# Kernel optimization log

Hardware: AMD Instinct MI355X
Metric: run time of the kernel (lower is better)

Reference implementation:

```python
import jax, jax.numpy as jnp
import numpy as np

B, N, E, H, ET = 1, 50000, 600000, 128, 8
EPS = 1e-5


def setup_inputs() -> dict:
    key = jax.random.key(0)
    ks = jax.random.split(key, 20)
    s = 1.0 / np.sqrt(H)
    s2 = 1.0 / np.sqrt(2 * H)
    u = lambda k, shape, b: jax.random.uniform(k, shape, jnp.float32, -b, b)
    return {
        "hidden": jax.random.normal(ks[0], (B, N, H), jnp.float32),
        "edge_index": jax.random.randint(ks[1], (2, E), 0, N),
        "edge_type": jax.random.randint(ks[2], (E,), 0, ET),
        "edge_emb": jax.random.normal(ks[3], (ET, H), jnp.float32),
        "Wq": u(ks[4], (H, H), s), "bq": u(ks[5], (H,), s),
        "Wk": u(ks[6], (H, H), s), "bk": u(ks[7], (H,), s),
        "Wv": u(ks[8], (H, H), s), "bv": u(ks[9], (H,), s),
        "Web": u(ks[10], (H, 1), s), "beb": u(ks[11], (1,), s),
        "W1": u(ks[12], (2 * H, H), s2), "b1": u(ks[13], (H,), s2),
        "W2": u(ks[14], (H, H), s), "b2": u(ks[15], (H,), s),
        "gamma": jnp.ones((H,), jnp.float32),
        "beta": jnp.zeros((H,), jnp.float32),
    }


def reference(hidden, edge_index, edge_type, edge_emb, Wq, bq, Wk, bk, Wv, bv,
              Web, beb, W1, b1, W2, b2, gamma, beta):
    source, target = edge_index[0], edge_index[1]
    src_h = hidden[:, source]                      # [B,E,H] gather
    tgt_h = hidden[:, target]                      # [B,E,H] gather
    eh = edge_emb[edge_type]                       # [E,H]

    q = tgt_h @ Wq + bq                            # [B,E,H]
    sk = src_h + eh[None]                          # [B,E,H]
    k = sk @ Wk + bk
    v = sk @ Wv + bv

    logits = (q * k).sum(-1) / np.sqrt(H)          # [B,E]
    logits = logits + (eh @ Web + beb)[:, 0][None] # edge bias, same across batch

    # segment softmax over incoming edges per target node
    lt = logits.T                                  # [E,B]
    mx = jax.ops.segment_max(lt, target, num_segments=N)   # [N,B]
    ex = jnp.exp(lt - mx[target])
    sm = jax.ops.segment_sum(ex, target, num_segments=N)   # [N,B]
    w = (ex / sm[target]).T                        # [B,E]

    messages = v * w[..., None]                    # [B,E,H]
    agg = jax.ops.segment_sum(jnp.moveaxis(messages, 1, 0), target,
                              num_segments=N)      # [N,B,H]
    agg = jnp.moveaxis(agg, 0, 1)                  # [B,N,H]

    h = jnp.concatenate([hidden, agg], axis=-1)    # [B,N,2H]
    upd = jax.nn.silu(h @ W1 + b1) @ W2 + b2

    x = hidden + upd
    mu = x.mean(-1, keepdims=True)
    var = ((x - mu) ** 2).mean(-1, keepdims=True)
    return (x - mu) / jnp.sqrt(var + EPS) * gamma + beta
```

## Files before the change

### kernel.cpp

```cpp
#include <hip/hip_runtime.h>
#include <math.h>

#define NN 50000
#define NPAD 50048
#define NTILES 3128
#define NE 600000
#define H 128
#define ET 8
#define EPS 1e-5f
#define INVSQ 0.08838834764831845f

typedef __attribute__((ext_vector_type(8))) short bf16x8;
typedef __attribute__((ext_vector_type(8))) unsigned short u16x8;
typedef __attribute__((ext_vector_type(4))) float f32x4;

static __device__ inline float bf_lo(unsigned int w) { return __uint_as_float(w << 16); }
static __device__ inline float bf_hi(unsigned int w) { return __uint_as_float(w & 0xFFFF0000u); }
static __device__ inline float bfu(unsigned short v) {
  return __uint_as_float((unsigned int)v << 16);
}
static __device__ inline unsigned short f2bf(float f) {
  unsigned int u = __float_as_uint(f);
  return (unsigned short)((u + 0x7FFFu + ((u >> 16) & 1u)) >> 16);
}

#define PH_B 3125
#define PW_B 384
#define ET_B 8
#define HIST_B 2344

__global__ __launch_bounds__(256) void prep_all_kernel(
    const float* __restrict__ hidden, const float* __restrict__ edge_emb,
    const float* __restrict__ Wq, const float* __restrict__ Wk, const float* __restrict__ Wv,
    const float* __restrict__ W1, const float* __restrict__ W2,
    const float* __restrict__ Web, const float* __restrict__ beb,
    const int* __restrict__ tgt,
    unsigned short* __restrict__ hcat, unsigned short* __restrict__ WqkvT,
    unsigned short* __restrict__ W1T, unsigned short* __restrict__ W2T,
    float* __restrict__ Kef, float* __restrict__ Vef, float* __restrict__ ebuf,
    int* __restrict__ deg) {
  const int blk = blockIdx.x;
  const int t = threadIdx.x;
  if (blk < PH_B) {
    int g = blk * 256 + t;
    int row = g >> 4, seg = g & 15;
    const float4* src = (const float4*)(hidden + (size_t)row * 128 + seg * 8);
    float4 x0 = src[0], x1 = src[1];
    u16x8 o;
    o[0] = f2bf(x0.x); o[1] = f2bf(x0.y); o[2] = f2bf(x0.z); o[3] = f2bf(x0.w);
    o[4] = f2bf(x1.x); o[5] = f2bf(x1.y); o[6] = f2bf(x1.z); o[7] = f2bf(x1.w);
    *(u16x8*)(hcat + (size_t)row * 256 + seg * 8) = o;
  } else if (blk < PH_B + PW_B) {
    int idx = (blk - PH_B) * 256 + t;
    if (idx < 49152) {
      int r = idx >> 7, k = idx & 127;
      const float* W = (r < 128) ? Wq : (r < 256) ? Wk : Wv;
      WqkvT[idx] = f2bf(W[k * 128 + (r & 127)]);
    } else if (idx < 81920) {
      int j = idx - 49152;
      int r = j >> 8, k = j & 255;
      W1T[j] = f2bf(W1[k * 128 + r]);
    } else if (idx < 98304) {
      int j = idx - 81920;
      int r = j >> 7, k = j & 127;
      W2T[j] = f2bf(W2[k * 128 + r]);
    }
  } else if (blk < PH_B + PW_B + ET_B) {
    int e = blk - (PH_B + PW_B);
    if (t < 128) {
      float sk = 0.f, sv = 0.f;
      for (int i = 0; i < 128; ++i) {
        float ev = edge_emb[e * 128 + i];
        sk = fmaf(ev, Wk[i * 128 + t], sk);
        sv = fmaf(ev, Wv[i * 128 + t], sv);
      }
      Kef[e * 128 + t] = sk;
      Vef[e * 128 + t] = sv;
    } else if (t == 128) {
      float s2 = beb[0];
      for (int i = 0; i < 128; ++i) s2 = fmaf(edge_emb[e * 128 + i], Web[i], s2);
      ebuf[e] = s2;
    }
  } else {
    int e = (blk - (PH_B + PW_B + ET_B)) * 256 + t;
    if (e < NE) atomicAdd(&deg[tgt[e]], 1);
  }
}

__global__ __launch_bounds__(512) void qkv_mfma_kernel(
    const unsigned short* __restrict__ hcat, const unsigned short* __restrict__ WqkvT,
    const float* __restrict__ bq, const float* __restrict__ bk, const float* __restrict__ bv,
    unsigned short* __restrict__ Qb, unsigned short* __restrict__ KV_u16) {
  __shared__ unsigned short stage[64][392];
  const int tid = threadIdx.x;
  const int w = tid >> 6, l = tid & 63;
  const int wr = w >> 2, wc = w & 3;
  const int lr = l & 15, lg = l >> 4;
  const int blk = blockIdx.x;

  f32x4 acc[2][6] = {};
  const unsigned short* Ab = hcat + (size_t)(blk * 64 + wr * 32 + lr) * 256 + lg * 8;
  const unsigned short* Bb = WqkvT + (size_t)(wc * 96 + lr) * 128 + lg * 8;
#pragma unroll
  for (int ks = 0; ks < 4; ++ks) {
    bf16x8 a0 = *(const bf16x8*)(Ab + ks * 32);
    bf16x8 a1 = *(const bf16x8*)(Ab + 16 * 256 + ks * 32);
#pragma unroll
    for (int ct = 0; ct < 6; ++ct) {
      bf16x8 b = *(const bf16x8*)(Bb + ct * 16 * 128 + ks * 32);
      acc[0][ct] = __builtin_amdgcn_mfma_f32_16x16x32_bf16(a0, b, acc[0][ct], 0, 0, 0);
      acc[1][ct] = __builtin_amdgcn_mfma_f32_16x16x32_bf16(a1, b, acc[1][ct], 0, 0, 0);
    }
  }
#pragma unroll
  for (int ct = 0; ct < 6; ++ct) {
    int c = wc * 96 + ct * 16 + lr;
    float bias = (c < 128) ? bq[c] : (c < 256) ? bk[c - 128] : bv[c - 256];
    float sc = (c < 128) ? INVSQ : 1.f;
    int off;
    if (c < 128) off = c;
    else if (c < 256) { int j = c - 128; off = 128 + ((j >> 1) << 2) + (j & 1); }
    else { int j = c - 256; off = 128 + ((j >> 1) << 2) + 2 + (j & 1); }
#pragma unroll
    for (int mt = 0; mt < 2; ++mt)
#pragma unroll
      for (int j = 0; j < 4; ++j)
        stage[wr * 32 + mt * 16 + lg * 4 + j][off] = f2bf((acc[mt][ct][j] + bias) * sc);
  }
  __syncthreads();
  for (int idx = tid; idx < 64 * 48; idx += 512) {
    int r = idx / 48, g = idx % 48;
    int row = blk * 64 + r;
    if (row >= NN) continue;
    u16x8 v = *(const u16x8*)(&stage[r][g * 8]);
    if (g < 16) *(u16x8*)(Qb + (size_t)row * 128 + g * 8) = v;
    else *(u16x8*)(KV_u16 + (size_t)row * 256 + (g - 16) * 8) = v;
  }
}

__global__ __launch_bounds__(256) void qke_kernel(const unsigned short* __restrict__ Qb,
                                                  const float* __restrict__ Kef,
                                                  const float* __restrict__ ebuf,
                                                  float* __restrict__ qke) {
  const int wid = (blockIdx.x * 256 + threadIdx.x) >> 6;
  const int lane = threadIdx.x & 63;
  const int et = lane >> 3, part = lane & 7;
  const unsigned short* q = Qb + (size_t)wid * 128 + part * 16;
  u16x8 q0 = *(const u16x8*)q;
  u16x8 q1 = *(const u16x8*)(q + 8);
  const float4* kf = (const float4*)(Kef + et * 128 + part * 16);
  float4 k0 = kf[0], k1 = kf[1], k2 = kf[2], k3 = kf[3];
  float d = 0.f;
  d = fmaf(bfu(q0[0]), k0.x, d); d = fmaf(bfu(q0[1]), k0.y, d);
  d = fmaf(bfu(q0[2]), k0.z, d); d = fmaf(bfu(q0[3]), k0.w, d);
  d = fmaf(bfu(q0[4]), k1.x, d); d = fmaf(bfu(q0[5]), k1.y, d);
  d = fmaf(bfu(q0[6]), k1.z, d); d = fmaf(bfu(q0[7]), k1.w, d);
  d = fmaf(bfu(q1[0]), k2.x, d); d = fmaf(bfu(q1[1]), k2.y, d);
  d = fmaf(bfu(q1[2]), k2.z, d); d = fmaf(bfu(q1[3]), k2.w, d);
  d = fmaf(bfu(q1[4]), k3.x, d); d = fmaf(bfu(q1[5]), k3.y, d);
  d = fmaf(bfu(q1[6]), k3.z, d); d = fmaf(bfu(q1[7]), k3.w, d);
#pragma unroll
  for (int o = 4; o >= 1; o >>= 1) d += __shfl_xor(d, o);
  if (part == 0) qke[(size_t)wid * 8 + et] = d + ebuf[et];
}

__global__ __launch_bounds__(256) void scan1_kernel(const int* __restrict__ deg,
                                                    int* __restrict__ excl,
                                                    int* __restrict__ sums) {
  __shared__ int buf[256];
  int idx = blockIdx.x * 256 + threadIdx.x;
  int v = (idx < NN) ? deg[idx] : 0;
  buf[threadIdx.x] = v;
  __syncthreads();
  for (int o = 1; o < 256; o <<= 1) {
    int tv = (threadIdx.x >= o) ? buf[threadIdx.x - o] : 0;
    __syncthreads();
    buf[threadIdx.x] += tv;
    __syncthreads();
  }
  if (idx < NN) excl[idx] = buf[threadIdx.x] - v;
  if (threadIdx.x == 255) sums[blockIdx.x] = buf[255];
}

__global__ __launch_bounds__(256) void scan2_kernel(int* __restrict__ sums, int nb) {
  __shared__ int buf[256];
  int v = (threadIdx.x < nb) ? sums[threadIdx.x] : 0;
  buf[threadIdx.x] = v;
  __syncthreads();
  for (int o = 1; o < 256; o <<= 1) {
    int tv = (threadIdx.x >= o) ? buf[threadIdx.x - o] : 0;
    __syncthreads();
    buf[threadIdx.x] += tv;
    __syncthreads();
  }
  if (threadIdx.x < nb) sums[threadIdx.x] = buf[threadIdx.x] - v;
}

__global__ __launch_bounds__(256) void scan3_kernel(const int* __restrict__ excl,
                                                    const int* __restrict__ sums,
                                                    int* __restrict__ row_off,
                                                    int* __restrict__ cursor) {
  int idx = blockIdx.x * 256 + threadIdx.x;
  if (idx < NN) {
    int r = excl[idx] + sums[blockIdx.x];
    row_off[idx] = r;
    cursor[idx] = r;
  }
  if (idx == 0) row_off[NN] = NE;
}

__global__ void scatter_kernel(const int* __restrict__ src, const int* __restrict__ tgt,
                               const int* __restrict__ et, int* __restrict__ cursor,
                               int* __restrict__ packed) {
  int e = blockIdx.x * blockDim.x + threadIdx.x;
  if (e < NE) {
    int pos = atomicAdd(&cursor[tgt[e]], 1);
    packed[pos] = src[e] | (et[e] << 16);
  }
}

__global__ __launch_bounds__(256) void attn_kernel(
    const unsigned short* __restrict__ Qb, const uint4* __restrict__ KV4,
    const float* __restrict__ qke, const float* __restrict__ Vef,
    const int* __restrict__ row_off, const int* __restrict__ packed,
    unsigned short* __restrict__ hcat_u16) {
  const int wid = (blockIdx.x * blockDim.x + threadIdx.x) >> 6;
  const int lane = threadIdx.x & 63;
  const int g = lane >> 4, m = lane & 15;
  const int beg = row_off[wid], end = row_off[wid + 1];
  u16x8 qv = *(const u16x8*)(Qb + (size_t)wid * 128 + m * 8);
  float q[8];
#pragma unroll
  for (int j = 0; j < 8; ++j) q[j] = bfu(qv[j]);
  const float* qkb = qke + (size_t)wid * 8;
  float a[8] = {0.f, 0.f, 0.f, 0.f, 0.f, 0.f, 0.f, 0.f};
  float s = 0.f;
  for (int i = beg; i < end; i += 4) {
    int ii = i + g;
    bool valid = ii < end;
    int p = packed[valid ? ii : beg];
    int src = p & 0xFFFF, et = p >> 16;
    const uint4* row = KV4 + (size_t)src * 32 + m * 2;
    uint4 x0 = row[0], x1 = row[1];
    float d;
    d = bf_lo(x0.x) * q[0];
    d = fmaf(bf_hi(x0.x), q[1], d);
    d = fmaf(bf_lo(x0.z), q[2], d);
    d = fmaf(bf_hi(x0.z), q[3], d);
    d = fmaf(bf_lo(x1.x), q[4], d);
    d = fmaf(bf_hi(x1.x), q[5], d);
    d = fmaf(bf_lo(x1.z), q[6], d);
    d = fmaf(bf_hi(x1.z), q[7], d);
#pragma unroll
    for (int o = 8; o >= 1; o >>= 1) d += __shfl_xor(d, o);
    float pe = __expf(d + qkb[et]);
    pe = valid ? pe : 0.f;
    s += pe;
    const float4* vef = (const float4*)(Vef + et * 128 + m * 8);
    float4 v0 = vef[0], v1 = vef[1];
    a[0] = fmaf(pe, bf_lo(x0.y) + v0.x, a[0]);
    a[1] = fmaf(pe, bf_hi(x0.y) + v0.y, a[1]);
    a[2] = fmaf(pe, bf_lo(x0.w) + v0.z, a[2]);
    a[3] = fmaf(pe, bf_hi(x0.w) + v0.w, a[3]);
    a[4] = fmaf(pe, bf_lo(x1.y) + v1.x, a[4]);
    a[5] = fmaf(pe, bf_hi(x1.y) + v1.y, a[5]);
    a[6] = fmaf(pe, bf_lo(x1.w) + v1.z, a[6]);
    a[7] = fmaf(pe, bf_hi(x1.w) + v1.w, a[7]);
  }
#pragma unroll
  for (int o = 16; o <= 32; o <<= 1) {
    s += __shfl_xor(s, o);
#pragma unroll
    for (int j = 0; j < 8; ++j) a[j] += __shfl_xor(a[j], o);
  }
  if (g == 0) {
    float inv = (s > 0.f) ? 1.f / s : 0.f;
    u16x8 o;
#pragma unroll
    for (int j = 0; j < 8; ++j) o[j] = f2bf(a[j] * inv);
    *(u16x8*)(hcat_u16 + (size_t)wid * 256 + 128 + m * 8) = o;
  }
}

__global__ __launch_bounds__(512) void ffn_mfma_kernel(
    const unsigned short* __restrict__ hcat, const float* __restrict__ hidden,
    const unsigned short* __restrict__ W1T, const unsigned short* __restrict__ W2T,
    const float* __restrict__ b1, const float* __restrict__ b2,
    const float* __restrict__ gamma, const float* __restrict__ beta,
    float* __restrict__ out) {
  __shared__ unsigned short w1s[32768];
  __shared__ unsigned short w2s[16384];
  __shared__ unsigned short mids[8][2176];
  const int tid = threadIdx.x;
  const int w = tid >> 6, l = tid & 63;
  const int lr = l & 15, lg = l >> 4;

#pragma unroll
  for (int it = 0; it < 8; ++it) {
    int idx = it * 512 + tid;
    int c = idx >> 5, ks8 = idx & 31;
    u16x8 v = *(const u16x8*)(W1T + c * 256 + ks8 * 8);
    int byte = (c * 512 + ks8 * 16) ^ ((c & 7) << 4);
    *(u16x8*)((char*)w1s + byte) = v;
  }
#pragma unroll
  for (int it = 0; it < 4; ++it) {
    int idx = it * 512 + tid;
    int c = idx >> 4, ks8 = idx & 15;
    u16x8 v = *(const u16x8*)(W2T + c * 128 + ks8 * 8);
    int byte = (c * 256 + ks8 * 16) ^ ((c & 7) << 4);
    *(u16x8*)((char*)w2s + byte) = v;
  }
  __syncthreads();

  float bias1[8], bias2[8], ga[8], be[8];
#pragma unroll
  for (int ct = 0; ct < 8; ++ct) {
    int c = ct * 16 + lr;
    bias1[ct] = b1[c];
    bias2[ct] = b2[c];
    ga[ct] = gamma[c];
    be[ct] = beta[c];
  }
  unsigned short* midw = mids[w];
  const char* w1b = (const char*)w1s;
  const char* w2b = (const char*)w2s;

  for (int t = blockIdx.x * 8 + w; t < NTILES; t += 2048) {
    const unsigned short* Ab = hcat + (size_t)(t * 16 + lr) * 256 + lg * 8;
    bf16x8 a[8];
#pragma unroll
    for (int ks = 0; ks < 8; ++ks) a[ks] = *(const bf16x8*)(Ab + ks * 32);

    f32x4 acc[8] = {};
#pragma unroll
    for (int ks = 0; ks < 8; ++ks) {
#pragma unroll
      for (int ct = 0; ct < 8; ++ct) {
        int byte = ((ct * 16 + lr) * 512 + (lg * 8 + ks * 32) * 2) ^ ((lr & 7) << 4);
        bf16x8 b = *(const bf16x8*)(w1b + byte);
        acc[ct] = __builtin_amdgcn_mfma_f32_16x16x32_bf16(a[ks], b, acc[ct], 0, 0, 0);
      }
    }

    float res[8][4];
#pragma unroll
    for (int ct = 0; ct < 8; ++ct)
#pragma unroll
      for (int j = 0; j < 4; ++j) {
        int r = t * 16 + lg * 4 + j;
        res[ct][j] = (r < NN) ? hidden[(size_t)r * 128 + ct * 16 + lr] : 0.f;
      }

#pragma unroll
    for (int ct = 0; ct < 8; ++ct) {
      float bb = bias1[ct];
#pragma unroll
      for (int j = 0; j < 4; ++j) {
        float x = acc[ct][j] + bb;
        float sl = x / (1.f + __expf(-x));
        midw[(lg * 4 + j) * 136 + ct * 16 + lr] = f2bf(sl);
      }
    }
    asm volatile("s_waitcnt lgkmcnt(0)" ::: "memory");
    __builtin_amdgcn_sched_barrier(0);

    f32x4 acc2[8] = {};
#pragma unroll
    for (int ks = 0; ks < 4; ++ks) {
      bf16x8 a2 = *(const bf16x8*)(midw + lr * 136 + lg * 8 + ks * 32);
#pragma unroll
      for (int ct = 0; ct < 8; ++ct) {
        int byte = ((ct * 16 + lr) * 256 + (lg * 8 + ks * 32) * 2) ^ ((lr & 7) << 4);
        bf16x8 b = *(const bf16x8*)(w2b + byte);
        acc2[ct] = __builtin_amdgcn_mfma_f32_16x16x32_bf16(a2, b, acc2[ct], 0, 0, 0);
      }
    }

    float x[8][4];
#pragma unroll
    for (int ct = 0; ct < 8; ++ct)
#pragma unroll
      for (int j = 0; j < 4; ++j) x[ct][j] = acc2[ct][j] + bias2[ct] + res[ct][j];
#pragma unroll
    for (int j = 0; j < 4; ++j) {
      float s = 0.f, ss = 0.f;
#pragma unroll
      for (int ct = 0; ct < 8; ++ct) {
        s += x[ct][j];
        ss += x[ct][j] * x[ct][j];
      }
#pragma unroll
      for (int o = 8; o >= 1; o >>= 1) {
        s += __shfl_xor(s, o);
        ss += __shfl_xor(ss, o);
      }
      float mu = s * (1.f / 128.f);
      float inv = rsqrtf(ss * (1.f / 128.f) - mu * mu + EPS);
      int r = t * 16 + lg * 4 + j;
      if (r < NN) {
#pragma unroll
        for (int ct = 0; ct < 8; ++ct) {
          int c = ct * 16 + lr;
          out[(size_t)r * 128 + c] = (x[ct][j] - mu) * inv * ga[ct] + be[ct];
        }
      }
    }
  }
}

extern "C" void kernel_launch(void* const* d_in, const int* in_sizes, int n_in,
                              void* d_out, int out_size, void* d_ws, size_t ws_size,
                              hipStream_t stream) {
  const float* hidden = (const float*)d_in[0];
  const int* edge_index = (const int*)d_in[1];
  const int* edge_type = (const int*)d_in[2];
  const float* edge_emb = (const float*)d_in[3];
  const float* Wq = (const float*)d_in[4];
  const float* bq = (const float*)d_in[5];
  const float* Wk = (const float*)d_in[6];
  const float* bk = (const float*)d_in[7];
  const float* Wv = (const float*)d_in[8];
  const float* bv = (const float*)d_in[9];
  const float* Web = (const float*)d_in[10];
  const float* beb = (const float*)d_in[11];
  const float* W1 = (const float*)d_in[12];
  const float* b1 = (const float*)d_in[13];
  const float* W2 = (const float*)d_in[14];
  const float* b2 = (const float*)d_in[15];
  const float* gamma = (const float*)d_in[16];
  const float* beta = (const float*)d_in[17];
  float* out = (float*)d_out;

  const int* srcp = edge_index;
  const int* tgtp = edge_index + NE;

  size_t off = 0;
  auto alloc = [&](size_t bytes) {
    void* p = (char*)d_ws + off;
    off += (bytes + 255) & ~(size_t)255;
    return p;
  };
  unsigned short* hcat = (unsigned short*)alloc((size_t)NPAD * 256 * 2);
  unsigned short* Qb = (unsigned short*)alloc((size_t)NPAD * 128 * 2);
  unsigned short* KV = (unsigned short*)alloc((size_t)NPAD * 256 * 2);
  unsigned short* WqkvT = (unsigned short*)alloc(384 * 128 * 2);
  unsigned short* W1T = (unsigned short*)alloc(128 * 256 * 2);
  unsigned short* W2T = (unsigned short*)alloc(128 * 128 * 2);
  float* Kef = (float*)alloc(ET * H * 4);
  float* Vef = (float*)alloc(ET * H * 4);
  float* ebuf = (float*)alloc(ET * 4);
  float* qke = (float*)alloc((size_t)NN * 8 * 4);
  int* deg = (int*)alloc((size_t)NN * 4);
  int* excl = (int*)alloc((size_t)NN * 4);
  int* sums = (int*)alloc(256 * 4);
  int* row_off = (int*)alloc((size_t)(NN + 1) * 4);
  int* cursor = (int*)alloc((size_t)NN * 4);
  int* packed = (int*)alloc((size_t)NE * 4);

  hipMemsetAsync(deg, 0, (size_t)NN * 4, stream);

  const int scan_blocks = (NN + 255) / 256;

  prep_all_kernel<<<PH_B + PW_B + ET_B + HIST_B, 256, 0, stream>>>(
      hidden, edge_emb, Wq, Wk, Wv, W1, W2, Web, beb, tgtp, hcat, WqkvT, W1T, W2T, Kef, Vef,
      ebuf, deg);
  scan1_kernel<<<scan_blocks, 256, 0, stream>>>(deg, excl, sums);
  scan2_kernel<<<1, 256, 0, stream>>>(sums, scan_blocks);
  scan3_kernel<<<scan_blocks, 256, 0, stream>>>(excl, sums, row_off, cursor);
  scatter_kernel<<<(NE + 255) / 256, 256, 0, stream>>>(srcp, tgtp, edge_type, cursor, packed);
  qkv_mfma_kernel<<<NPAD / 64, 512, 0, stream>>>(hcat, WqkvT, bq, bk, bv, Qb, KV);
  qke_kernel<<<NN / 4, 256, 0, stream>>>(Qb, Kef, ebuf, qke);
  attn_kernel<<<(NN * 64) / 256, 256, 0, stream>>>(Qb, (const uint4*)KV, qke, Vef, row_off,
                                                   packed, hcat);
  ffn_mfma_kernel<<<256, 512, 0, stream>>>(hcat, hidden, W1T, W2T, b1, b2, gamma, beta, out);
}
```

Measured before the change: 296.7 us.

## Fuse qke into QKV kernel, unroll attention edges by two, widen FFN blocks

Computes the per-node q·Kef edge-type dot products inside the QKV MFMA kernel from the staged Q tile in shared memory, removing the separate qke launch and its Q reload. The attention loop now handles two edge groups per iteration so more gathers are in flight. The FFN kernel goes from 8 to 12 waves per block, with grid-stride and weight-load loops adjusted to match. Risks include higher register pressure in attention, lower occupancy for the 768-thread FFN block given its large LDS footprint, and a scalar per-thread Kef loop that is not vectorised.

After: 340.9 us. 1.15x slower.

```diff
diff --git a/kernel.cpp b/kernel.cpp
--- a/kernel.cpp
+++ b/kernel.cpp
@@ -90,7 +90,9 @@
 __global__ __launch_bounds__(512) void qkv_mfma_kernel(
     const unsigned short* __restrict__ hcat, const unsigned short* __restrict__ WqkvT,
     const float* __restrict__ bq, const float* __restrict__ bk, const float* __restrict__ bv,
-    unsigned short* __restrict__ Qb, unsigned short* __restrict__ KV_u16) {
+    const float* __restrict__ Kef, const float* __restrict__ ebuf,
+    unsigned short* __restrict__ Qb, unsigned short* __restrict__ KV_u16,
+    float* __restrict__ qke) {
   __shared__ unsigned short stage[64][392];
   const int tid = threadIdx.x;
   const int w = tid >> 6, l = tid & 63;
@@ -136,32 +138,22 @@
     if (g < 16) *(u16x8*)(Qb + (size_t)row * 128 + g * 8) = v;
     else *(u16x8*)(KV_u16 + (size_t)row * 256 + (g - 16) * 8) = v;
   }
-}
-
-__global__ __launch_bounds__(256) void qke_kernel(const unsigned short* __restrict__ Qb,
-                                                  const float* __restrict__ Kef,
-                                                  const float* __restrict__ ebuf,
-                                                  float* __restrict__ qke) {
-  const int wid = (blockIdx.x * 256 + threadIdx.x) >> 6;
-  const int lane = threadIdx.x & 63;
-  const int et = lane >> 3, part = lane & 7;
-  const unsigned short* q = Qb + (size_t)wid * 128 + part * 16;
-  u16x8 q0 = *(const u16x8*)q;
-  u16x8 q1 = *(const u16x8*)(q + 8);
-  const float4* kf = (const float4*)(Kef + et * 128 + part * 16);
-  float4 k0 = kf[0], k1 = kf[1], k2 = kf[2], k3 = kf[3];
-  float d = 0.f;
-  d = fmaf(bfu(q0[0]), k0.x, d); d = fmaf(bfu(q0[1]), k0.y, d);
-  d = fmaf(bfu(q0[2]), k0.z, d); d = fmaf(bfu(q0[3]), k0.w, d);
-  d = fmaf(bfu(q0[4]), k1.x, d); d = fmaf(bfu(q0[5]), k1.y, d);
-  d = fmaf(bfu(q0[6]), k1.z, d); d = fmaf(bfu(q0[7]), k1.w, d);
-  d = fmaf(bfu(q1[0]), k2.x, d); d = fmaf(bfu(q1[1]), k2.y, d);
-  d = fmaf(bfu(q1[2]), k2.z, d); d = fmaf(bfu(q1[3]), k2.w, d);
-  d = fmaf(bfu(q1[4]), k3.x, d); d = fmaf(bfu(q1[5]), k3.y, d);
-  d = fmaf(bfu(q1[6]), k3.z, d); d = fmaf(bfu(q1[7]), k3.w, d);
-#pragma unroll
-  for (int o = 4; o >= 1; o >>= 1) d += __shfl_xor(d, o);
-  if (part == 0) qke[(size_t)wid * 8 + et] = d + ebuf[et];
+  {
+    int row = tid >> 3, et = tid & 7;
+    int node = blk * 64 + row;
+    if (node < NN) {
+      const float* kf = Kef + et * 128;
+      const unsigned short* qs = &stage[row][0];
+      float d = 0.f;
+#pragma unroll 16
+      for (int c = 0; c < 128; c += 2) {
+        unsigned int w2 = *(const unsigned int*)(qs + c);
+        d = fmaf(bf_lo(w2), kf[c], d);
+        d = fmaf(bf_hi(w2), kf[c + 1], d);
+      }
+      qke[(size_t)node * 8 + et] = d + ebuf[et];
+    }
+  }
 }
 
 __global__ __launch_bounds__(256) void scan1_kernel(const int* __restrict__ deg,
@@ -235,37 +227,64 @@
   const float* qkb = qke + (size_t)wid * 8;
   float a[8] = {0.f, 0.f, 0.f, 0.f, 0.f, 0.f, 0.f, 0.f};
   float s = 0.f;
-  for (int i = beg; i < end; i += 4) {
-    int ii = i + g;
-    bool valid = ii < end;
-    int p = packed[valid ? ii : beg];
-    int src = p & 0xFFFF, et = p >> 16;
-    const uint4* row = KV4 + (size_t)src * 32 + m * 2;
-    uint4 x0 = row[0], x1 = row[1];
-    float d;
-    d = bf_lo(x0.x) * q[0];
-    d = fmaf(bf_hi(x0.x), q[1], d);
-    d = fmaf(bf_lo(x0.z), q[2], d);
-    d = fmaf(bf_hi(x0.z), q[3], d);
-    d = fmaf(bf_lo(x1.x), q[4], d);
-    d = fmaf(bf_hi(x1.x), q[5], d);
-    d = fmaf(bf_lo(x1.z), q[6], d);
-    d = fmaf(bf_hi(x1.z), q[7], d);
-#pragma unroll
-    for (int o = 8; o >= 1; o >>= 1) d += __shfl_xor(d, o);
-    float pe = __expf(d + qkb[et]);
-    pe = valid ? pe : 0.f;
-    s += pe;
-    const float4* vef = (const float4*)(Vef + et * 128 + m * 8);
-    float4 v0 = vef[0], v1 = vef[1];
-    a[0] = fmaf(pe, bf_lo(x0.y) + v0.x, a[0]);
-    a[1] = fmaf(pe, bf_hi(x0.y) + v0.y, a[1]);
-    a[2] = fmaf(pe, bf_lo(x0.w) + v0.z, a[2]);
-    a[3] = fmaf(pe, bf_hi(x0.w) + v0.w, a[3]);
-    a[4] = fmaf(pe, bf_lo(x1.y) + v1.x, a[4]);
-    a[5] = fmaf(pe, bf_hi(x1.y) + v1.y, a[5]);
-    a[6] = fmaf(pe, bf_lo(x1.w) + v1.z, a[6]);
-    a[7] = fmaf(pe, bf_hi(x1.w) + v1.w, a[7]);
+  for (int i = beg; i < end; i += 8) {
+    int iA = i + g, iB = i + 4 + g;
+    bool vA = iA < end, vB = iB < end;
+    int pA = packed[vA ? iA : beg];
+    int pB = packed[vB ? iB : beg];
+    int sA = pA & 0xFFFF, eA = pA >> 16;
+    int sB = pB & 0xFFFF, eB = pB >> 16;
+    const uint4* rowA = KV4 + (size_t)sA * 32 + m * 2;
+    const uint4* rowB = KV4 + (size_t)sB * 32 + m * 2;
+    uint4 xA0 = rowA[0], xA1 = rowA[1];
+    uint4 xB0 = rowB[0], xB1 = rowB[1];
+    float dA, dB;
+    dA = bf_lo(xA0.x) * q[0];
+    dB = bf_lo(xB0.x) * q[0];
+    dA = fmaf(bf_hi(xA0.x), q[1], dA);
+    dB = fmaf(bf_hi(xB0.x), q[1], dB);
+    dA = fmaf(bf_lo(xA0.z), q[2], dA);
+    dB = fmaf(bf_lo(xB0.z), q[2], dB);
+    dA = fmaf(bf_hi(xA0.z), q[3], dA);
+    dB = fmaf(bf_hi(xB0.z), q[3], dB);
+    dA = fmaf(bf_lo(xA1.x), q[4], dA);
+    dB = fmaf(bf_lo(xB1.x), q[4], dB);
+    dA = fmaf(bf_hi(xA1.x), q[5], dA);
+    dB = fmaf(bf_hi(xB1.x), q[5], dB);
+    dA = fmaf(bf_lo(xA1.z), q[6], dA);
+    dB = fmaf(bf_lo(xB1.z), q[6], dB);
+    dA = fmaf(bf_hi(xA1.z), q[7], dA);
+    dB = fmaf(bf_hi(xB1.z), q[7], dB);
+#pragma unroll
+    for (int o = 8; o >= 1; o >>= 1) {
+      dA += __shfl_xor(dA, o);
+      dB += __shfl_xor(dB, o);
+    }
+    float peA = __expf(dA + qkb[eA]);
+    float peB = __expf(dB + qkb[eB]);
+    peA = vA ? peA : 0.f;
+    peB = vB ? peB : 0.f;
+    s += peA + peB;
+    const float4* vefA = (const float4*)(Vef + eA * 128 + m * 8);
+    const float4* vefB = (const float4*)(Vef + eB * 128 + m * 8);
+    float4 vA0 = vefA[0], vA1 = vefA[1];
+    float4 vB0 = vefB[0], vB1 = vefB[1];
+    a[0] = fmaf(peA, bf_lo(xA0.y) + vA0.x, a[0]);
+    a[1] = fmaf(peA, bf_hi(xA0.y) + vA0.y, a[1]);
+    a[2] = fmaf(peA, bf_lo(xA0.w) + vA0.z, a[2]);
+    a[3] = fmaf(peA, bf_hi(xA0.w) + vA0.w, a[3]);
+    a[4] = fmaf(peA, bf_lo(xA1.y) + vA1.x, a[4]);
+    a[5] = fmaf(peA, bf_hi(xA1.y) + vA1.y, a[5]);
+    a[6] = fmaf(peA, bf_lo(xA1.w) + vA1.z, a[6]);
+    a[7] = fmaf(peA, bf_hi(xA1.w) + vA1.w, a[7]);
+    a[0] = fmaf(peB, bf_lo(xB0.y) + vB0.x, a[0]);
+    a[1] = fmaf(peB, bf_hi(xB0.y) + vB0.y, a[1]);
+    a[2] = fmaf(peB, bf_lo(xB0.w) + vB0.z, a[2]);
+    a[3] = fmaf(peB, bf_hi(xB0.w) + vB0.w, a[3]);
+    a[4] = fmaf(peB, bf_lo(xB1.y) + vB1.x, a[4]);
+    a[5] = fmaf(peB, bf_hi(xB1.y) + vB1.y, a[5]);
+    a[6] = fmaf(peB, bf_lo(xB1.w) + vB1.z, a[6]);
+    a[7] = fmaf(peB, bf_hi(xB1.w) + vB1.w, a[7]);
   }
 #pragma unroll
   for (int o = 16; o <= 32; o <<= 1) {
@@ -282,7 +301,7 @@
   }
 }
 
-__global__ __launch_bounds__(512) void ffn_mfma_kernel(
+__global__ __launch_bounds__(768) void ffn_mfma_kernel(
     const unsigned short* __restrict__ hcat, const float* __restrict__ hidden,
     const unsigned short* __restrict__ W1T, const unsigned short* __restrict__ W2T,
     const float* __restrict__ b1, const float* __restrict__ b2,
@@ -290,26 +309,30 @@
     float* __restrict__ out) {
   __shared__ unsigned short w1s[32768];
   __shared__ unsigned short w2s[16384];
-  __shared__ unsigned short mids[8][2176];
+  __shared__ unsigned short mids[12][2176];
   const int tid = threadIdx.x;
   const int w = tid >> 6, l = tid & 63;
   const int lr = l & 15, lg = l >> 4;
 
 #pragma unroll
-  for (int it = 0; it < 8; ++it) {
-    int idx = it * 512 + tid;
-    int c = idx >> 5, ks8 = idx & 31;
-    u16x8 v = *(const u16x8*)(W1T + c * 256 + ks8 * 8);
-    int byte = (c * 512 + ks8 * 16) ^ ((c & 7) << 4);
-    *(u16x8*)((char*)w1s + byte) = v;
-  }
-#pragma unroll
-  for (int it = 0; it < 4; ++it) {
-    int idx = it * 512 + tid;
-    int c = idx >> 4, ks8 = idx & 15;
-    u16x8 v = *(const u16x8*)(W2T + c * 128 + ks8 * 8);
-    int byte = (c * 256 + ks8 * 16) ^ ((c & 7) << 4);
-    *(u16x8*)((char*)w2s + byte) = v;
+  for (int it = 0; it < 6; ++it) {
+    int idx = it * 768 + tid;
+    if (idx < 4096) {
+      int c = idx >> 5, ks8 = idx & 31;
+      u16x8 v = *(const u16x8*)(W1T + c * 256 + ks8 * 8);
+      int byte = (c * 512 + ks8 * 16) ^ ((c & 7) << 4);
+      *(u16x8*)((char*)w1s + byte) = v;
+    }
+  }
+#pragma unroll
+  for (int it = 0; it < 3; ++it) {
+    int idx = it * 768 + tid;
+    if (idx < 2048) {
+      int c = idx >> 4, ks8 = idx & 15;
+      u16x8 v = *(const u16x8*)(W2T + c * 128 + ks8 * 8);
+      int byte = (c * 256 + ks8 * 16) ^ ((c & 7) << 4);
+      *(u16x8*)((char*)w2s + byte) = v;
+    }
   }
   __syncthreads();
 
@@ -326,7 +349,7 @@
   const char* w1b = (const char*)w1s;
   const char* w2b = (const char*)w2s;
 
-  for (int t = blockIdx.x * 8 + w; t < NTILES; t += 2048) {
+  for (int t = blockIdx.x * 12 + w; t < NTILES; t += 3072) {
     const unsigned short* Ab = hcat + (size_t)(t * 16 + lr) * 256 + lg * 8;
     bf16x8 a[8];
 #pragma unroll
@@ -469,9 +492,9 @@
   scan2_kernel<<<1, 256, 0, stream>>>(sums, scan_blocks);
   scan3_kernel<<<scan_blocks, 256, 0, stream>>>(excl, sums, row_off, cursor);
   scatter_kernel<<<(NE + 255) / 256, 256, 0, stream>>>(srcp, tgtp, edge_type, cursor, packed);
-  qkv_mfma_kernel<<<NPAD / 64, 512, 0, stream>>>(hcat, WqkvT, bq, bk, bv, Qb, KV);
-  qke_kernel<<<NN / 4, 256, 0, stream>>>(Qb, Kef, ebuf, qke);
+  qkv_mfma_kernel<<<NPAD / 64, 512, 0, stream>>>(hcat, WqkvT, bq, bk, bv, Kef, ebuf, Qb, KV,
+                                                 qke);
   attn_kernel<<<(NN * 64) / 256, 256, 0, stream>>>(Qb, (const uint4*)KV, qke, Vef, row_off,
                                                    packed, hcat);
-  ffn_mfma_kernel<<<256, 512, 0, stream>>>(hcat, hidden, W1T, W2T, b1, b2, gamma, beta, out);
-}
+  ffn_mfma_kernel<<<256, 768, 0, stream>>>(hcat, hidden, W1T, W2T, b1, b2, gamma, beta, out);
+}
```
